# Optimization experiments

Hardware: AMD Instinct MI355X
Metric: run time of the kernel (lower is better)

The kernel has to match this reference:

```python
import jax, jax.numpy as jnp
import numpy as np

GS_ITERS = 10
GS_TAU = 0.5
NEG = -1e9
B, L, D, H = 4, 512, 64, 128


def gphi_scores(x, W1, b1, W2, b2):
    # Faithful to: concat([x_i, x_j]) -> Linear(2D,H) -> ReLU -> Linear(H,1).squeeze(-1)
    # Linear on the concat of [x_i, x_j] == x_i @ W1[:D] + x_j @ W1[D:] (fused, no [B,L,L,2D] tensor).
    d = x.shape[-1]
    pi = jnp.einsum('bld,dh->blh', x, W1[:d])   # row-index half of concat
    pj = jnp.einsum('bld,dh->blh', x, W1[d:])   # col-index half of concat
    h = jax.nn.relu(pi[:, :, None, :] + pj[:, None, :, :] + b1)  # [B,L,L,H]
    return jnp.einsum('blmh,h->blm', h, W2[:, 0]) + b2[0]        # [B,L,L]


def gumbel_sinkhorn(log_alpha, gumbel, pad_mask, tau, n_iters):
    # (scores + gumbel noise)/tau, mask padded rows/cols, alternate row/col log-normalization.
    la = (log_alpha + gumbel) / tau
    la = jnp.where(pad_mask, NEG, la)

    def step(la, _):
        la = la - jax.nn.logsumexp(la, axis=2, keepdims=True)  # row normalize
        la = la - jax.nn.logsumexp(la, axis=1, keepdims=True)  # col normalize
        la = jnp.where(pad_mask, NEG, la)
        return la, None

    la, _ = jax.lax.scan(step, la, None, length=n_iters)
    return jnp.exp(la)


def make_pad_mask(seq_lens, max_len):
    # mask_map logic: for a sequence of length s, rows < s have cols < s valid; rows >= s fully invalid.
    ar = jnp.arange(max_len)
    s = seq_lens[:, None, None]
    valid = (ar[None, :, None] < s) & (ar[None, None, :] < s)
    return ~valid  # True where gumbel-masked


def setup_inputs() -> dict:
    key = jax.random.key(0)
    ks = jax.random.split(key, 8)
    event_time = jax.random.uniform(ks[0], (B, L), dtype=jnp.float32) * 10.0
    event_type = jax.random.randint(ks[1], (B, L), 0, 50, dtype=jnp.int32)
    clean_enc_out = jax.random.normal(ks[2], (B, L, D), dtype=jnp.float32)
    seq_lens = jax.random.randint(ks[3], (B,), 1, L + 1, dtype=jnp.int32)
    u = jax.random.uniform(ks[4], (B, L, L), dtype=jnp.float32, minval=1e-6, maxval=1.0 - 1e-6)
    gumbel_noise = -jnp.log(-jnp.log(u))
    # gphi_mlp params (xavier-ish scaling)
    W1 = jax.random.normal(ks[5], (2 * D, H), dtype=jnp.float32) * (1.0 / np.sqrt(2 * D))
    b1 = jnp.full((H,), 0.01, dtype=jnp.float32)
    W2 = jax.random.normal(ks[6], (H, 1), dtype=jnp.float32) * (1.0 / np.sqrt(H))
    b2 = jnp.full((1,), 0.01, dtype=jnp.float32)
    return {"event_time": event_time, "event_type": event_type,
            "clean_enc_out": clean_enc_out, "seq_lens": seq_lens,
            "gumbel_noise": gumbel_noise, "W1": W1, "b1": b1, "W2": W2, "b2": b2}


def reference(event_time, event_type, clean_enc_out, seq_lens, gumbel_noise, W1, b1, W2, b2):
    pad_mask = make_pad_mask(seq_lens, event_time.shape[1])
    scores = gphi_scores(clean_enc_out, W1, b1, W2, b2)           # [B,L,L]
    perm = gumbel_sinkhorn(scores, gumbel_noise, pad_mask, GS_TAU, GS_ITERS)
    # same_perm_matrix=True, no_time_noise=True path
    types_permed = jnp.einsum('bl,blm->bm', event_type.astype(jnp.float32), perm)
    times_permed = jnp.einsum('bl,blm->bm', event_time, perm)
    return types_permed, times_permed, perm
```

## Files before the change

kernel.cpp:

```cpp
#include <hip/hip_runtime.h>
#include <cstdint>

#define BB 4
#define LL 512
#define DD 64
#define HH 128
#define NEGV -1000000000.0f
#define NBLK 256
#define NTHR 1024
#define NACT 64

union U8 { unsigned long long u; float2 f; };

__device__ __forceinline__ float2 cload_f2(const float* p) {
    U8 v;
    v.u = __hip_atomic_load((const unsigned long long*)p,
                            __ATOMIC_RELAXED, __HIP_MEMORY_SCOPE_AGENT);
    return v.f;
}
__device__ __forceinline__ void cstore_f2(float* p, float2 x) {
    U8 v; v.f = x;
    __hip_atomic_store((unsigned long long*)p, v.u,
                       __ATOMIC_RELAXED, __HIP_MEMORY_SCOPE_AGENT);
}

__device__ __forceinline__ void grid_barrier(unsigned* cnt, unsigned target) {
    __builtin_amdgcn_fence(__ATOMIC_RELEASE, "workgroup");
    __syncthreads();
    if (threadIdx.x == 0) {
        __hip_atomic_fetch_add(cnt, 1u, __ATOMIC_RELAXED, __HIP_MEMORY_SCOPE_AGENT);
        while (__hip_atomic_load(cnt, __ATOMIC_RELAXED, __HIP_MEMORY_SCOPE_AGENT) < target)
            __builtin_amdgcn_s_sleep(1);
    }
    __builtin_amdgcn_fence(__ATOMIC_ACQUIRE, "workgroup");
    __syncthreads();
}

__device__ __forceinline__ float hmax4(float4 v) {
    return fmaxf(fmaxf(v.x, v.y), fmaxf(v.z, v.w));
}

__global__ __launch_bounds__(NTHR) void mega(
    const float* __restrict__ etime, const int* __restrict__ etype,
    const float* __restrict__ x, const int* __restrict__ slens,
    const float* __restrict__ gum, const float* __restrict__ W1,
    const float* __restrict__ b1, const float* __restrict__ W2,
    const float* __restrict__ b2, float* __restrict__ out, float* __restrict__ ws)
{
    __shared__ float smem[19072];

    unsigned* cntA = (unsigned*)ws;
    unsigned* cntB = (unsigned*)ws + 32;
    float* piG   = ws + 64;
    float* pjG   = piG + BB * LL * HH;
    float* laG   = pjG + BB * LL * HH;
    float* cpkG  = laG + (size_t)BB * LL * LL;
    float* poutG = cpkG + 2 * BB * 32 * LL * 2;

    const int t = threadIdx.x;
    const int bx = blockIdx.x;

    {
        int gid = (bx << 10) + t;
        int arr = gid >> 17;
        int rem = gid & 131071;
        int row = rem >> 6;
        int h0  = (rem & 63) << 1;
        const float* xr = x + row * DD;
        const float* wb = W1 + (size_t)(arr * DD) * HH + h0;
        float a0 = arr ? 0.f : b1[h0];
        float a1 = arr ? 0.f : b1[h0 + 1];
        #pragma unroll 8
        for (int d = 0; d < DD; ++d) {
            float xv = xr[d];
            a0 = fmaf(xv, wb[d * HH + 0], a0);
            a1 = fmaf(xv, wb[d * HH + 1], a1);
        }
        float* dst = (arr ? pjG : piG) + (size_t)row * HH + h0;
        cstore_f2(dst, make_float2(a0, a1));
    }
    grid_barrier(cntA, 1 * NBLK);

    {
        float* sp  = smem;
        float* sq  = smem + 8192;
        float* sw2 = smem + 18944;
        int jt = bx & 7, it8 = (bx >> 3) & 7, b = bx >> 6;
        int i0 = it8 << 6, j0 = jt << 6;
        int rowb = b * LL + i0, colb = b * LL + j0;

        #pragma unroll
        for (int k = 0; k < 8; ++k) {
            int idx = (k << 10) + t;
            int buf = idx >> 12;
            int u   = idx & 4095;
            int row = u >> 6;
            int du  = u & 63;
            int q   = du >> 1;
            int hi  = du & 1;
            int dq  = q ^ ((row >> 2) & 7);
            const float* src = (buf ? pjG + (size_t)(colb + row) * HH
                                    : piG + (size_t)(rowb + row) * HH) + (du << 1);
            float2 v = cload_f2(src);
            float* dst = (buf ? sq : sp) + row * HH + (dq << 2) + (hi << 1);
            *(float2*)dst = v;
        }
        if (t < HH) sw2[t] = W2[t];
        __syncthreads();

        int hg = t >> 8, tt = t & 255;
        int w = tt >> 6, lane = tt & 63;
        int ti = ((w >> 1) << 3) + (lane >> 3);
        int tj = ((w & 1) << 3) + (lane & 7);
        int kti = ti & 7, ktj = tj & 7;

        float acc[4][4];
        #pragma unroll
        for (int a = 0; a < 4; ++a)
            #pragma unroll
            for (int c = 0; c < 4; ++c) acc[a][c] = 0.f;

        for (int hq = hg * 8; hq < hg * 8 + 8; ++hq) {
            float4 w4 = *(const float4*)(sw2 + (hq << 2));
            int offi = (hq ^ kti) << 2;
            int offj = (hq ^ ktj) << 2;
            float4 pa[4], pb[4];
            #pragma unroll
            for (int a = 0; a < 4; ++a) pa[a] = *(const float4*)(sp + (4*ti + a) * HH + offi);
            #pragma unroll
            for (int c = 0; c < 4; ++c) pb[c] = *(const float4*)(sq + (4*tj + c) * HH + offj);
            #pragma unroll
            for (int a = 0; a < 4; ++a) {
                #pragma unroll
                for (int c = 0; c < 4; ++c) {
                    float t0 = fmaxf(pa[a].x + pb[c].x, 0.f);
                    float t1 = fmaxf(pa[a].y + pb[c].y, 0.f);
                    float t2 = fmaxf(pa[a].z + pb[c].z, 0.f);
                    float t3 = fmaxf(pa[a].w + pb[c].w, 0.f);
                    float s = acc[a][c];
                    s += t0 * w4.x; s += t1 * w4.y; s += t2 * w4.z; s += t3 * w4.w;
                    acc[a][c] = s;
                }
            }
        }
        __syncthreads();
        float* cbuf = smem;
        #pragma unroll
        for (int a = 0; a < 4; ++a)
            #pragma unroll
            for (int c = 0; c < 4; ++c)
                cbuf[(((hg << 8) + tt) << 4) + (a << 2) + c] = acc[a][c];
        __syncthreads();

        int tt2 = t >> 2, a2 = t & 3;
        int w2_ = tt2 >> 6, lane2 = tt2 & 63;
        int ti2 = ((w2_ >> 1) << 3) + (lane2 >> 3);
        int tj2 = ((w2_ & 1) << 3) + (lane2 & 7);
        float4 o = make_float4(0.f, 0.f, 0.f, 0.f);
        #pragma unroll
        for (int g = 0; g < 4; ++g) {
            float4 pp = *(const float4*)(cbuf + (((g << 8) + tt2) << 4) + (a2 << 2));
            o.x += pp.x; o.y += pp.y; o.z += pp.z; o.w += pp.w;
        }
        int sl = slens[b];
        float bb2 = b2[0];
        int ig = i0 + 4 * ti2 + a2;
        int jb = j0 + 4 * tj2;
        float4 g4 = *(const float4*)(gum + ((size_t)(b * LL + ig)) * LL + jb);
        bool iv = ig < sl;
        float4 res;
        res.x = (iv && (jb + 0) < sl) ? (o.x + bb2 + g4.x) * 2.0f : NEGV;
        res.y = (iv && (jb + 1) < sl) ? (o.y + bb2 + g4.y) * 2.0f : NEGV;
        res.z = (iv && (jb + 2) < sl) ? (o.z + bb2 + g4.z) * 2.0f : NEGV;
        res.w = (iv && (jb + 3) < sl) ? (o.w + bb2 + g4.w) * 2.0f : NEGV;
        float* lap = laG + ((size_t)(b * LL + ig)) * LL + jb;
        cstore_f2(lap,     make_float2(res.x, res.y));
        cstore_f2(lap + 2, make_float2(res.z, res.w));
    }
    grid_barrier(cntA, 2 * NBLK);

    if (bx >= NACT) return;

    const int b2i = bx >> 4;
    const int stripe = bx & 15;
    const int r0 = stripe << 5;
    float* sla  = smem;
    float* redm = smem + 16384;
    float* reds = smem + 17408;
    float* clse = smem + 18432;
    const int sl_a = slens[b2i];
    float tyv = 0.f, tmv = 0.f;

    {
        const float* src = laG + (((size_t)(b2i << 9) + r0) << 9);
        #pragma unroll
        for (int k = 0; k < 8; ++k) {
            int u = (k << 10) + t;
            float2 v = cload_f2(src + (u << 1));
            *(float2*)(sla + (u << 1)) = v;
        }
        __syncthreads();
    }

    for (int it = 0; it < 10; ++it) {
        const int par = it & 1;
        const int last = (it == 9);
        {
            int r = t >> 5, cq = t & 31;
            float4 v[4];
            #pragma unroll
            for (int k = 0; k < 4; ++k)
                v[k] = *(float4*)(sla + (r << 9) + ((cq + (k << 5)) << 2));
            float m = fmaxf(fmaxf(hmax4(v[0]), hmax4(v[1])), fmaxf(hmax4(v[2]), hmax4(v[3])));
            #pragma unroll
            for (int off = 16; off; off >>= 1) m = fmaxf(m, __shfl_xor(m, off));
            float s = 0.f;
            #pragma unroll
            for (int k = 0; k < 4; ++k)
                s += __expf(v[k].x - m) + __expf(v[k].y - m) + __expf(v[k].z - m) + __expf(v[k].w - m);
            #pragma unroll
            for (int off = 16; off; off >>= 1) s += __shfl_xor(s, off);
            float lse = m + __logf(s);
            #pragma unroll
            for (int k = 0; k < 4; ++k) {
                v[k].x -= lse; v[k].y -= lse; v[k].z -= lse; v[k].w -= lse;
                *(float4*)(sla + (r << 9) + ((cq + (k << 5)) << 2)) = v[k];
            }
            __syncthreads();

            int c = t & 511, half = t >> 9;
            float vv[16];
            #pragma unroll
            for (int rr = 0; rr < 16; ++rr) vv[rr] = sla[(((half << 4) + rr) << 9) + c];
            float mp = vv[0];
            #pragma unroll
            for (int rr = 1; rr < 16; ++rr) mp = fmaxf(mp, vv[rr]);
            float spv = 0.f;
            #pragma unroll
            for (int rr = 0; rr < 16; ++rr) spv += __expf(vv[rr] - mp);
            size_t pidx = ((((size_t)par * BB + b2i) << 5) + (stripe << 1) + half) * LL + c;
            cstore_f2(cpkG + pidx * 2, make_float2(mp, spv));
        }
        grid_barrier(cntB, (it + 1) * NACT);
        {
            int c = t & 511, half = t >> 9;
            const float* pB = cpkG + (((((size_t)par * BB + b2i) << 5)) * LL) * 2;
            int g0 = half << 4;
            float mreg[16], sreg[16];
            #pragma unroll
            for (int g = 0; g < 16; ++g) {
                float2 ms = cload_f2(pB + (size_t)((g0 + g) * LL + c) * 2);
                mreg[g] = ms.x; sreg[g] = ms.y;
            }
            float M = mreg[0];
            #pragma unroll
            for (int g = 1; g < 16; ++g) M = fmaxf(M, mreg[g]);
            redm[(half << 9) + c] = M;
            __syncthreads();
            float Mg = fmaxf(redm[c], redm[512 + c]);
            float S = 0.f;
            #pragma unroll
            for (int g = 0; g < 16; ++g)
                S = fmaf(sreg[g], __expf(mreg[g] - Mg), S);
            reds[(half << 9) + c] = S;
            __syncthreads();
            if (half == 0) clse[c] = Mg + __logf(reds[c] + reds[512 + c]);
            __syncthreads();

            int r = t >> 5, cq = t & 31;
            int grow = r0 + r;
            bool ivR = grow < sl_a;
            if (!last) {
                #pragma unroll
                for (int k = 0; k < 4; ++k) {
                    int cb = (cq + (k << 5)) << 2;
                    float4 v = *(float4*)(sla + (r << 9) + cb);
                    float4 l = *(const float4*)(clse + cb);
                    float4 o;
                    o.x = (ivR && (cb + 0) < sl_a) ? v.x - l.x : NEGV;
                    o.y = (ivR && (cb + 1) < sl_a) ? v.y - l.y : NEGV;
                    o.z = (ivR && (cb + 2) < sl_a) ? v.z - l.z : NEGV;
                    o.w = (ivR && (cb + 3) < sl_a) ? v.w - l.w : NEGV;
                    *(float4*)(sla + (r << 9) + cb) = o;
                }
            } else {
                float etf = (float)etype[(b2i << 9) + grow];
                float etv = etime[(b2i << 9) + grow];
                float4 p[4];
                #pragma unroll
                for (int k = 0; k < 4; ++k) {
                    int cb = (cq + (k << 5)) << 2;
                    float4 v = *(float4*)(sla + (r << 9) + cb);
                    float4 l = *(const float4*)(clse + cb);
                    float4 q;
                    q.x = (ivR && (cb + 0) < sl_a) ? __expf(v.x - l.x) : 0.f;
                    q.y = (ivR && (cb + 1) < sl_a) ? __expf(v.y - l.y) : 0.f;
                    q.z = (ivR && (cb + 2) < sl_a) ? __expf(v.z - l.z) : 0.f;
                    q.w = (ivR && (cb + 3) < sl_a) ? __expf(v.w - l.w) : 0.f;
                    p[k] = q;
                    *(float4*)(out + 2 * BB * LL + (((size_t)(b2i << 9) + grow) << 9) + cb) = q;
                }
                #pragma unroll
                for (int k = 0; k < 4; ++k) {
                    int cb = (cq + (k << 5)) << 2;
                    *(float4*)(sla + (r << 9) + cb) =
                        make_float4(p[k].x * etf, p[k].y * etf, p[k].z * etf, p[k].w * etf);
                }
                __syncthreads();
                {
                    int c2 = t & 511, h2 = t >> 9;
                    float sA = 0.f;
                    #pragma unroll
                    for (int rr = 0; rr < 16; ++rr) sA += sla[(((h2 << 4) + rr) << 9) + c2];
                    redm[(h2 << 9) + c2] = sA;
                }
                __syncthreads();
                if (t < 512) tyv = redm[t] + redm[512 + t];
                __syncthreads();
                #pragma unroll
                for (int k = 0; k < 4; ++k) {
                    int cb = (cq + (k << 5)) << 2;
                    *(float4*)(sla + (r << 9) + cb) =
                        make_float4(p[k].x * etv, p[k].y * etv, p[k].z * etv, p[k].w * etv);
                }
                __syncthreads();
                {
                    int c2 = t & 511, h2 = t >> 9;
                    float sB = 0.f;
                    #pragma unroll
                    for (int rr = 0; rr < 16; ++rr) sB += sla[(((h2 << 4) + rr) << 9) + c2];
                    reds[(h2 << 9) + c2] = sB;
                }
                __syncthreads();
                if (t < 512) {
                    tmv = reds[t] + reds[512 + t];
                    cstore_f2(poutG + (size_t)(((b2i << 4) + stripe) * LL + t) * 2,
                              make_float2(tyv, tmv));
                }
            }
        }
    }
    grid_barrier(cntB, 11 * NACT);

    if (t < 32) {
        int b = bx >> 4, chunk = bx & 15;
        int c = (chunk << 5) + t;
        float a = 0.f, d = 0.f;
        #pragma unroll
        for (int s = 0; s < 16; ++s) {
            float2 p = cload_f2(poutG + (size_t)(((b << 4) + s) * LL + c) * 2);
            a += p.x; d += p.y;
        }
        out[(b << 9) + c] = a;
        out[BB * LL + (b << 9) + c] = d;
    }
}

extern "C" void kernel_launch(void* const* d_in, const int* in_sizes, int n_in,
                              void* d_out, int out_size, void* d_ws, size_t ws_size,
                              hipStream_t stream)
{
    const float* etime = (const float*)d_in[0];
    const int*   etype = (const int*)d_in[1];
    const float* x     = (const float*)d_in[2];
    const int*   slens = (const int*)d_in[3];
    const float* gum   = (const float*)d_in[4];
    const float* W1    = (const float*)d_in[5];
    const float* b1    = (const float*)d_in[6];
    const float* W2    = (const float*)d_in[7];
    const float* b2    = (const float*)d_in[8];
    float* out = (float*)d_out;
    float* wsf = (float*)d_ws;

    hipMemsetAsync(d_ws, 0, 256, stream);

    void* args[] = {(void*)&etime, (void*)&etype, (void*)&x, (void*)&slens, (void*)&gum,
                    (void*)&W1, (void*)&b1, (void*)&W2, (void*)&b2, (void*)&out, (void*)&wsf};
    hipError_t err = hipLaunchCooperativeKernel((const void*)mega, dim3(NBLK), dim3(NTHR),
                                                args, 0, stream);
    if (err != hipSuccess) {
        mega<<<NBLK, NTHR, 0, stream>>>(etime, etype, x, slens, gum, W1, b1, W2, b2, out, wsf);
    }
}
```

Baseline: 139.4 us.

## Use per-batch barriers and pre-merge column partials inside block for Sinkhorn

The Sinkhorn phase now syncs only the 16 blocks that share a batch element, each batch using its own counter, instead of all 64 active blocks on one counter. Each block also merges its two half-stripe column (max, sum) partials in shared memory before publishing, which halves the partial-buffer traffic and the loads after the barrier. The goal is lower barrier latency and less global traffic per iteration, at the cost of an extra __syncthreads and a larger zeroed counter region.

```diff
diff --git a/kernel.cpp b/kernel.cpp
--- a/kernel.cpp
+++ b/kernel.cpp
@@ -50,12 +50,11 @@
     __shared__ float smem[19072];
 
     unsigned* cntA = (unsigned*)ws;
-    unsigned* cntB = (unsigned*)ws + 32;
-    float* piG   = ws + 64;
+    float* piG   = ws + 128;
     float* pjG   = piG + BB * LL * HH;
     float* laG   = pjG + BB * LL * HH;
     float* cpkG  = laG + (size_t)BB * LL * LL;
-    float* poutG = cpkG + 2 * BB * 32 * LL * 2;
+    float* poutG = cpkG + (size_t)2 * BB * 16 * LL * 2;
 
     const int t = threadIdx.x;
     const int bx = blockIdx.x;
@@ -184,6 +183,7 @@
     const int b2i = bx >> 4;
     const int stripe = bx & 15;
     const int r0 = stripe << 5;
+    unsigned* cntB = (unsigned*)ws + 16 + (b2i << 4);
     float* sla  = smem;
     float* redm = smem + 16384;
     float* reds = smem + 17408;
@@ -238,31 +238,39 @@
             float spv = 0.f;
             #pragma unroll
             for (int rr = 0; rr < 16; ++rr) spv += __expf(vv[rr] - mp);
-            size_t pidx = ((((size_t)par * BB + b2i) << 5) + (stripe << 1) + half) * LL + c;
-            cstore_f2(cpkG + pidx * 2, make_float2(mp, spv));
-        }
-        grid_barrier(cntB, (it + 1) * NACT);
+            redm[(half << 9) + c] = mp;
+            reds[(half << 9) + c] = spv;
+            __syncthreads();
+            if (half == 0) {
+                float m1 = redm[512 + c], s1 = reds[512 + c];
+                float M = fmaxf(mp, m1);
+                float S = fmaf(spv, __expf(mp - M), s1 * __expf(m1 - M));
+                cstore_f2(cpkG + (size_t)(((((par * BB) + b2i) << 4) + stripe) * LL + c) * 2,
+                          make_float2(M, S));
+            }
+        }
+        grid_barrier(cntB, (it + 1) * 16);
         {
             int c = t & 511, half = t >> 9;
-            const float* pB = cpkG + (((((size_t)par * BB + b2i) << 5)) * LL) * 2;
-            int g0 = half << 4;
-            float mreg[16], sreg[16];
-            #pragma unroll
-            for (int g = 0; g < 16; ++g) {
+            const float* pB = cpkG + (size_t)((((par * BB) + b2i) << 4) * LL) * 2;
+            int g0 = half << 3;
+            float mreg[8], sreg[8];
+            #pragma unroll
+            for (int g = 0; g < 8; ++g) {
                 float2 ms = cload_f2(pB + (size_t)((g0 + g) * LL + c) * 2);
                 mreg[g] = ms.x; sreg[g] = ms.y;
             }
-            float M = mreg[0];
-            #pragma unroll
-            for (int g = 1; g < 16; ++g) M = fmaxf(M, mreg[g]);
-            redm[(half << 9) + c] = M;
+            float M8 = mreg[0];
+            #pragma unroll
+            for (int g = 1; g < 8; ++g) M8 = fmaxf(M8, mreg[g]);
+            redm[(half << 9) + c] = M8;
             __syncthreads();
             float Mg = fmaxf(redm[c], redm[512 + c]);
-            float S = 0.f;
-            #pragma unroll
-            for (int g = 0; g < 16; ++g)
-                S = fmaf(sreg[g], __expf(mreg[g] - Mg), S);
-            reds[(half << 9) + c] = S;
+            float S8 = 0.f;
+            #pragma unroll
+            for (int g = 0; g < 8; ++g)
+                S8 = fmaf(sreg[g], __expf(mreg[g] - Mg), S8);
+            reds[(half << 9) + c] = S8;
             __syncthreads();
             if (half == 0) clse[c] = Mg + __logf(reds[c] + reds[512 + c]);
             __syncthreads();
@@ -340,19 +348,18 @@
             }
         }
     }
-    grid_barrier(cntB, 11 * NACT);
+    grid_barrier(cntB, 11 * 16);
 
     if (t < 32) {
-        int b = bx >> 4, chunk = bx & 15;
-        int c = (chunk << 5) + t;
+        int c = (stripe << 5) + t;
         float a = 0.f, d = 0.f;
         #pragma unroll
         for (int s = 0; s < 16; ++s) {
-            float2 p = cload_f2(poutG + (size_t)(((b << 4) + s) * LL + c) * 2);
+            float2 p = cload_f2(poutG + (size_t)(((b2i << 4) + s) * LL + c) * 2);
             a += p.x; d += p.y;
         }
-        out[(b << 9) + c] = a;
-        out[BB * LL + (b << 9) + c] = d;
+        out[(b2i << 9) + c] = a;
+        out[BB * LL + (b2i << 9) + c] = d;
     }
 }
 
@@ -372,7 +379,7 @@
     float* out = (float*)d_out;
     float* wsf = (float*)d_ws;
 
-    hipMemsetAsync(d_ws, 0, 256, stream);
+    hipMemsetAsync(d_ws, 0, 512, stream);
 
     void* args[] = {(void*)&etime, (void*)&etype, (void*)&x, (void*)&slens, (void*)&gum,
                     (void*)&W1, (void*)&b1, (void*)&W2, (void*)&b2, (void*)&out, (void*)&wsf};
```

After: 125.3 us. -10.1%, faster.
